# Kernel optimization log

Measured on AMD Instinct MI355X. Metric: run time of the kernel, lower is better.

Reference implementation:

```python
import jax, jax.numpy as jnp
import numpy as np

B, S, HID = 4, 2048, 512
NH, HD = 8, 64
MAX_REL = 512


def setup_inputs() -> dict:
    key = jax.random.key(0)
    ks = jax.random.split(key, 10)
    sd = 0.02
    return {
        "hidden_states": jax.random.normal(ks[0], (B, S, HID), jnp.float32),
        "attention_mask": jnp.ones((B, S), jnp.float32),
        "Wq": jax.random.normal(ks[1], (HID, HID), jnp.float32) * sd,
        "bq": jnp.zeros((HID,), jnp.float32),
        "Wk": jax.random.normal(ks[2], (HID, HID), jnp.float32) * sd,
        "bk": jnp.zeros((HID,), jnp.float32),
        "Wv": jax.random.normal(ks[3], (HID, HID), jnp.float32) * sd,
        "bv": jnp.zeros((HID,), jnp.float32),
        "Wo": jax.random.normal(ks[4], (HID, HID), jnp.float32) * sd,
        "bo": jnp.zeros((HID,), jnp.float32),
        "rel_table": jax.random.normal(ks[5], (2 * MAX_REL + 1, NH), jnp.float32) * sd,
    }


def _heads(x):
    # [B,S,HID] -> [B,NH,S,HD]
    return x.reshape(B, S, NH, HD).transpose(0, 2, 1, 3)


def reference(hidden_states, attention_mask, Wq, bq, Wk, bk, Wv, bv, Wo, bo, rel_table):
    q = _heads(hidden_states @ Wq + bq)
    k = _heads(hidden_states @ Wk + bk)
    v = _heads(hidden_states @ Wv + bv)

    scores = jnp.einsum("bhqd,bhkd->bhqk", q, k) / jnp.sqrt(jnp.float32(HD))

    # relative position bias: rel[i,j] = clip(j-i, -MAX_REL, MAX_REL) + MAX_REL
    pos = jnp.arange(S)
    rel = jnp.clip(pos[None, :] - pos[:, None], -MAX_REL, MAX_REL) + MAX_REL
    bias = rel_table[rel]                      # [S,S,NH]
    bias = bias.transpose(2, 0, 1)             # [NH,S,S]
    scores = scores + bias[None]

    # mask: 1 attend, 0 masked
    neg = jnp.finfo(scores.dtype).min
    scores = scores + (1.0 - attention_mask)[:, None, None, :] * neg

    probs = jax.nn.softmax(scores, axis=-1)
    ctx = jnp.einsum("bhqk,bhkd->bhqd", probs, v)
    ctx = ctx.transpose(0, 2, 1, 3).reshape(B, S, HID)
    return ctx @ Wo + bo
```

## Files before the change

kernel.cpp:

```cpp
#include <hip/hip_runtime.h>
#include <hip/hip_bf16.h>

#define B_    4
#define S_    2048
#define HID_  512
#define NH_   8
#define HD_   64
#define MAXREL 512
#define M_    (B_ * S_)

#define LOG2E 1.44269504f
#define SCALE_Q (0.125f * LOG2E)

typedef __attribute__((ext_vector_type(8))) short bf8;
typedef __attribute__((ext_vector_type(4))) float f4;

static __device__ __forceinline__ unsigned short f2bf(float f) {
    union { float f; unsigned int u; } v; v.f = f;
    unsigned int u = v.u;
    unsigned int r = (u + 0x7FFFu + ((u >> 16) & 1u)) >> 16;
    return (unsigned short)r;
}

static __device__ __forceinline__ float ex2(float x) {
    float r; asm("v_exp_f32 %0, %1" : "=v"(r) : "v"(x)); return r;
}

#define MFMA16(a, b, c) __builtin_amdgcn_mfma_f32_16x16x32_bf16((a), (b), (c), 0, 0, 0)

__global__ void k_cast_hs(const float* __restrict__ src, unsigned short* __restrict__ dst, int n4) {
    int i = blockIdx.x * blockDim.x + threadIdx.x;
    if (i >= n4) return;
    float4 v = ((const float4*)src)[i];
    ushort4 o;
    o.x = f2bf(v.x); o.y = f2bf(v.y); o.z = f2bf(v.z); o.w = f2bf(v.w);
    ((ushort4*)dst)[i] = o;
}

__global__ void k_transpose_w4(const float* __restrict__ W0, const float* __restrict__ W1,
                               const float* __restrict__ W2, const float* __restrict__ W3,
                               unsigned short* __restrict__ T0, unsigned short* __restrict__ T1,
                               unsigned short* __restrict__ T2, unsigned short* __restrict__ T3) {
    __shared__ float tile[32][33];
    const int z = blockIdx.z;
    const float* W = (z == 0) ? W0 : (z == 1) ? W1 : (z == 2) ? W2 : W3;
    unsigned short* T = (z == 0) ? T0 : (z == 1) ? T1 : (z == 2) ? T2 : T3;
    const int tx = threadIdx.x & 31, ty = threadIdx.x >> 5;
    const int n0 = blockIdx.x * 32, k0 = blockIdx.y * 32;
    #pragma unroll
    for (int i = 0; i < 4; ++i)
        tile[ty + i * 8][tx] = W[(size_t)(k0 + ty + i * 8) * HID_ + n0 + tx];
    __syncthreads();
    #pragma unroll
    for (int i = 0; i < 4; ++i)
        T[(size_t)(n0 + ty + i * 8) * HID_ + k0 + tx] = f2bf(tile[tx][ty + i * 8]);
}

__global__ __launch_bounds__(256, 3) void k_gemm_qkv(
    const unsigned short* __restrict__ Abf,
    const unsigned short* __restrict__ Wqt, const unsigned short* __restrict__ Wkt,
    const unsigned short* __restrict__ Wvt,
    const float* __restrict__ bq, const float* __restrict__ bk, const float* __restrict__ bv,
    unsigned short* __restrict__ Q, unsigned short* __restrict__ K, unsigned short* __restrict__ Vt)
{
    __shared__ unsigned short Al[2][128 * 32];
    __shared__ unsigned short Bl[2][128 * 32];

    const int t = threadIdx.x;
    const int lane = t & 63, w = t >> 6;
    const int lr = lane & 15, lg = lane >> 4;
    const int wr = w >> 1, wc = w & 1;

    const int m0 = blockIdx.x * 128;
    const int ng = blockIdx.y * 128;
    const int z = ng >> 9;
    const int n0 = ng & 511;
    const unsigned short* Wt = (z == 0) ? Wqt : ((z == 1) ? Wkt : Wvt);
    const float* bias = (z == 0) ? bq : ((z == 1) ? bk : bv);
    const float osc = (z == 0) ? SCALE_Q : 1.0f;

    const int srow = t >> 2, skk = (t & 3) * 8;
    const int sslot = (t & 3) ^ ((srow >> 1) & 3);
    const int so0 = srow * 32 + sslot * 8;
    const int so1 = (srow + 64) * 32 + sslot * 8;
    const unsigned short* Ag = &Abf[(size_t)(m0 + srow) * HID_ + skk];
    const unsigned short* Bg = &Wt[(size_t)(n0 + srow) * HID_ + skk];

    const int fx = (lr >> 1) & 3;
    int aoff[4], boff[4];
    #pragma unroll
    for (int i = 0; i < 4; ++i) {
        aoff[i] = (wr * 64 + i * 16 + lr) * 32 + ((lg ^ fx) * 8);
        boff[i] = (wc * 64 + i * 16 + lr) * 32 + ((lg ^ fx) * 8);
    }

    {
        bf8 a0 = *(const bf8*)Ag;
        bf8 a1 = *(const bf8*)(Ag + (size_t)64 * HID_);
        bf8 b0 = *(const bf8*)Bg;
        bf8 b1 = *(const bf8*)(Bg + (size_t)64 * HID_);
        *(bf8*)&Al[0][so0] = a0;  *(bf8*)&Al[0][so1] = a1;
        *(bf8*)&Bl[0][so0] = b0;  *(bf8*)&Bl[0][so1] = b1;
    }
    __syncthreads();

    f4 acc[4][4] = {};
    for (int kt = 0; kt < 16; ++kt) {
        const int cur = kt & 1;
        bf8 ra0, ra1, rb0, rb1;
        if (kt < 15) {
            const int ko = (kt + 1) * 32;
            ra0 = *(const bf8*)(Ag + ko);
            ra1 = *(const bf8*)(Ag + (size_t)64 * HID_ + ko);
            rb0 = *(const bf8*)(Bg + ko);
            rb1 = *(const bf8*)(Bg + (size_t)64 * HID_ + ko);
        }
        bf8 af[4], bf_[4];
        #pragma unroll
        for (int i = 0; i < 4; ++i) {
            af[i]  = *(const bf8*)&Al[cur][aoff[i]];
            bf_[i] = *(const bf8*)&Bl[cur][boff[i]];
        }
        #pragma unroll
        for (int mi = 0; mi < 4; ++mi)
            #pragma unroll
            for (int ni = 0; ni < 4; ++ni)
                acc[mi][ni] = MFMA16(af[mi], bf_[ni], acc[mi][ni]);
        if (kt < 15) {
            const int nxt = cur ^ 1;
            *(bf8*)&Al[nxt][so0] = ra0;  *(bf8*)&Al[nxt][so1] = ra1;
            *(bf8*)&Bl[nxt][so0] = rb0;  *(bf8*)&Bl[nxt][so1] = rb1;
        }
        __syncthreads();
    }

    #pragma unroll
    for (int mi = 0; mi < 4; ++mi)
    #pragma unroll
    for (int ni = 0; ni < 4; ++ni) {
        const int col = n0 + wc * 64 + ni * 16 + lr;
        const int h = col >> 6, d = col & 63;
        const float bs = bias[col];
        const int row0 = m0 + wr * 64 + mi * 16 + lg * 4;
        const int b = row0 >> 11, s0 = row0 & 2047;
        if (z == 2) {
            ushort4 o;
            o.x = f2bf(acc[mi][ni][0] + bs);
            o.y = f2bf(acc[mi][ni][1] + bs);
            o.z = f2bf(acc[mi][ni][2] + bs);
            o.w = f2bf(acc[mi][ni][3] + bs);
            *(ushort4*)&Vt[(((size_t)(b * NH_ + h)) * HD_ + d) * S_ + s0] = o;
        } else {
            unsigned short* dst = (z == 0) ? Q : K;
            #pragma unroll
            for (int r = 0; r < 4; ++r) {
                float v = (acc[mi][ni][r] + bs) * osc;
                dst[(((size_t)(b * NH_ + h)) * S_ + s0 + r) * HD_ + d] = f2bf(v);
            }
        }
    }
}

__global__ __launch_bounds__(512) void k_gemm_out(
    const unsigned short* __restrict__ Abf,
    const unsigned short* __restrict__ Wot,
    const float* __restrict__ bo,
    float* __restrict__ out)
{
    __shared__ unsigned short Al[2][128 * 32];
    __shared__ unsigned short Bl[2][128 * 32];

    const int t = threadIdx.x;
    const int lane = t & 63, w = t >> 6;
    const int lr = lane & 15, lg = lane >> 4;
    const int wr = w >> 2, wc = w & 3;

    const int m0 = blockIdx.x * 128;
    const int n0 = blockIdx.y * 128;

    const int srow = t >> 2, skk = (t & 3) * 8;
    const int sslot = (t & 3) ^ ((srow >> 1) & 3);
    const int so = srow * 32 + sslot * 8;
    const unsigned short* Ag = &Abf[(size_t)(m0 + srow) * HID_ + skk];
    const unsigned short* Bg = &Wot[(size_t)(n0 + srow) * HID_ + skk];

    const int fx = (lr >> 1) & 3;
    int aoff[4], boff[2];
    #pragma unroll
    for (int i = 0; i < 4; ++i)
        aoff[i] = (wr * 64 + i * 16 + lr) * 32 + ((lg ^ fx) * 8);
    #pragma unroll
    for (int i = 0; i < 2; ++i)
        boff[i] = (wc * 32 + i * 16 + lr) * 32 + ((lg ^ fx) * 8);

    {
        bf8 a0 = *(const bf8*)Ag;
        bf8 b0 = *(const bf8*)Bg;
        *(bf8*)&Al[0][so] = a0;
        *(bf8*)&Bl[0][so] = b0;
    }
    __syncthreads();

    f4 acc[4][2] = {};
    for (int kt = 0; kt < 16; ++kt) {
        const int cur = kt & 1;
        bf8 ra, rb;
        if (kt < 15) {
            const int ko = (kt + 1) * 32;
            ra = *(const bf8*)(Ag + ko);
            rb = *(const bf8*)(Bg + ko);
        }
        bf8 af[4], bf_[2];
        #pragma unroll
        for (int i = 0; i < 4; ++i) af[i] = *(const bf8*)&Al[cur][aoff[i]];
        #pragma unroll
        for (int i = 0; i < 2; ++i) bf_[i] = *(const bf8*)&Bl[cur][boff[i]];
        #pragma unroll
        for (int mi = 0; mi < 4; ++mi)
            #pragma unroll
            for (int ni = 0; ni < 2; ++ni)
                acc[mi][ni] = MFMA16(af[mi], bf_[ni], acc[mi][ni]);
        if (kt < 15) {
            const int nxt = cur ^ 1;
            *(bf8*)&Al[nxt][so] = ra;
            *(bf8*)&Bl[nxt][so] = rb;
        }
        __syncthreads();
    }

    #pragma unroll
    for (int mi = 0; mi < 4; ++mi)
    #pragma unroll
    for (int ni = 0; ni < 2; ++ni) {
        const int col = n0 + wc * 32 + ni * 16 + lr;
        const float bs = bo[col];
        const int row0 = m0 + wr * 64 + mi * 16 + lg * 4;
        #pragma unroll
        for (int r = 0; r < 4; ++r)
            out[(size_t)(row0 + r) * HID_ + col] = acc[mi][ni][r] + bs;
    }
}

__global__ __launch_bounds__(512, 4) void k_flash(
    const unsigned short* __restrict__ Q, const unsigned short* __restrict__ K,
    const unsigned short* __restrict__ Vt,
    const float* __restrict__ rel_table, const float* __restrict__ mask,
    unsigned short* __restrict__ ctx)
{
    __shared__ unsigned short Klds[2][4096];
    __shared__ unsigned short Vlds[2][4096];
    __shared__ unsigned short Ps[8][16][72];
    __shared__ float maskc[S_];
    __shared__ float Tb[1028];

    const int t = threadIdx.x;
    const int lane = t & 63, w = t >> 6;
    const int lr = lane & 15, lg = lane >> 4;

    const int flat = blockIdx.x;
    const int idx = flat >> 3;
    const int bh = (flat & 7) * 4 + (idx >> 4);
    const int qb = idx & 15;
    const int b = bh >> 3, h = bh & 7;
    const int q0 = qb * 128;

    for (int i = t; i < 1025; i += 512) Tb[i] = rel_table[i * NH_ + h] * LOG2E;
    for (int i = t; i < S_; i += 512)
        maskc[i] = (1.0f - mask[b * S_ + i]) * -3.0e38f;

    const unsigned short* Kb = K + (size_t)bh * S_ * HD_;
    const unsigned short* Vb = Vt + (size_t)bh * HD_ * S_;

    const int myq = q0 + w * 16 + lr;
    bf8 qf0, qf1;
    {
        const unsigned short* qg = &Q[((size_t)bh * S_ + myq) * HD_ + lg * 8];
        qf0 = *(const bf8*)qg;
        qf1 = *(const bf8*)(qg + 32);
    }

    const int srow = t >> 3, sslot = t & 7;
    const int ldso = srow * 64 + ((sslot ^ (srow & 7)) * 8);

    f4 cacc[4] = {};
    float m_s = -INFINITY, l_s = 0.f;

    {
        bf8 a = *(const bf8*)&Kb[(size_t)srow * HD_ + sslot * 8];
        bf8 d = *(const bf8*)&Vb[(size_t)srow * S_ + sslot * 8];
        *(bf8*)&Klds[0][ldso] = a;
        *(bf8*)&Vlds[0][ldso] = d;
    }
    __syncthreads();

    const int xr = lr & 7;
    for (int ti = 0; ti < 32; ++ti) {
        const int cur = ti & 1;
        const int kv0 = ti * 64;

        bf8 sK, sV;
        if (ti < 31) {
            const int nx = kv0 + 64;
            sK = *(const bf8*)&Kb[(size_t)(nx + srow) * HD_ + sslot * 8];
            sV = *(const bf8*)&Vb[(size_t)srow * S_ + nx + sslot * 8];
        }

        f4 sa[4];
        #pragma unroll
        for (int nt = 0; nt < 4; ++nt) {
            const int row = (nt * 16 + lr) * 64;
            bf8 kf0 = *(const bf8*)&Klds[cur][row + ((0 + lg) ^ xr) * 8];
            bf8 kf1 = *(const bf8*)&Klds[cur][row + ((4 + lg) ^ xr) * 8];
            f4 u = {};
            u = MFMA16(kf0, qf0, u);
            u = MFMA16(kf1, qf1, u);
            sa[nt] = u;
        }

        float4 mk[4];
        #pragma unroll
        for (int nt = 0; nt < 4; ++nt)
            mk[nt] = *(const float4*)&maskc[kv0 + nt * 16 + lg * 4];

        float tmax = -INFINITY;
        #pragma unroll
        for (int nt = 0; nt < 4; ++nt) {
            const int kb0 = kv0 + nt * 16 + lg * 4 - myq + MAXREL;
            #pragma unroll
            for (int r = 0; r < 4; ++r) {
                int ic = kb0 + r;
                ic = ic < 0 ? 0 : (ic > 2 * MAXREL ? 2 * MAXREL : ic);
                float mkv = (r == 0) ? mk[nt].x : (r == 1) ? mk[nt].y : (r == 2) ? mk[nt].z : mk[nt].w;
                float sv = sa[nt][r] + Tb[ic] + mkv;
                sa[nt][r] = sv;
                tmax = fmaxf(tmax, sv);
            }
        }
        tmax = fmaxf(tmax, __shfl_xor(tmax, 16));
        tmax = fmaxf(tmax, __shfl_xor(tmax, 32));

        if (!__all(tmax <= m_s + 8.0f)) {
            const float mnew = fmaxf(m_s, tmax);
            const float fac = ex2(m_s - mnew);
            l_s *= fac;
            #pragma unroll
            for (int dt = 0; dt < 4; ++dt)
                #pragma unroll
                for (int r = 0; r < 4; ++r) cacc[dt][r] *= fac;
            m_s = mnew;
        }

        float psum = 0.f;
        unsigned int pk[8];
        #pragma unroll
        for (int nt = 0; nt < 4; ++nt) {
            float p0 = ex2(sa[nt][0] - m_s);
            float p1 = ex2(sa[nt][1] - m_s);
            float p2 = ex2(sa[nt][2] - m_s);
            float p3 = ex2(sa[nt][3] - m_s);
            psum += (p0 + p1) + (p2 + p3);
            asm("v_cvt_pk_bf16_f32 %0, %1, %2" : "=v"(pk[nt * 2])     : "v"(p0), "v"(p1));
            asm("v_cvt_pk_bf16_f32 %0, %1, %2" : "=v"(pk[nt * 2 + 1]) : "v"(p2), "v"(p3));
        }
        psum += __shfl_xor(psum, 16);
        psum += __shfl_xor(psum, 32);
        l_s += psum;

        #pragma unroll
        for (int nt = 0; nt < 4; ++nt) {
            uint2 pv; pv.x = pk[nt * 2]; pv.y = pk[nt * 2 + 1];
            *(uint2*)&Ps[w][lr][nt * 16 + lg * 4] = pv;
        }
        asm volatile("s_waitcnt lgkmcnt(0)" ::: "memory");
        __builtin_amdgcn_sched_barrier(0);

        #pragma unroll
        for (int kc = 0; kc < 2; ++kc) {
            bf8 pb = *(const bf8*)&Ps[w][lr][kc * 32 + lg * 8];
            #pragma unroll
            for (int dt = 0; dt < 4; ++dt) {
                const int row = (dt * 16 + lr) * 64;
                bf8 vf = *(const bf8*)&Vlds[cur][row + ((kc * 4 + lg) ^ xr) * 8];
                cacc[dt] = MFMA16(vf, pb, cacc[dt]);
            }
        }

        if (ti < 31) {
            *(bf8*)&Klds[cur ^ 1][ldso] = sK;
            *(bf8*)&Vlds[cur ^ 1][ldso] = sV;
        }
        __syncthreads();
    }

    const float inv = 1.0f / l_s;
    unsigned short* cg = &ctx[(size_t)(b * S_ + myq) * HID_ + h * HD_];
    #pragma unroll
    for (int dt = 0; dt < 4; ++dt) {
        ushort4 o;
        o.x = f2bf(cacc[dt][0] * inv);
        o.y = f2bf(cacc[dt][1] * inv);
        o.z = f2bf(cacc[dt][2] * inv);
        o.w = f2bf(cacc[dt][3] * inv);
        *(ushort4*)&cg[dt * 16 + lg * 4] = o;
    }
}

extern "C" void kernel_launch(void* const* d_in, const int* in_sizes, int n_in,
                              void* d_out, int out_size, void* d_ws, size_t ws_size,
                              hipStream_t stream) {
    const float* hs  = (const float*)d_in[0];
    const float* msk = (const float*)d_in[1];
    const float* Wq  = (const float*)d_in[2];
    const float* bq  = (const float*)d_in[3];
    const float* Wk  = (const float*)d_in[4];
    const float* bk  = (const float*)d_in[5];
    const float* Wv  = (const float*)d_in[6];
    const float* bv  = (const float*)d_in[7];
    const float* Wo  = (const float*)d_in[8];
    const float* bo  = (const float*)d_in[9];
    const float* rel = (const float*)d_in[10];
    float* out = (float*)d_out;

    char* ws = (char*)d_ws;
    unsigned short* hsb = (unsigned short*)ws; ws += (size_t)M_ * HID_ * 2;
    unsigned short* Wqt = (unsigned short*)ws; ws += (size_t)HID_ * HID_ * 2;
    unsigned short* Wkt = (unsigned short*)ws; ws += (size_t)HID_ * HID_ * 2;
    unsigned short* Wvt = (unsigned short*)ws; ws += (size_t)HID_ * HID_ * 2;
    unsigned short* Wot = (unsigned short*)ws; ws += (size_t)HID_ * HID_ * 2;
    unsigned short* Qb  = (unsigned short*)ws; ws += (size_t)M_ * HID_ * 2;
    unsigned short* Kb  = (unsigned short*)ws; ws += (size_t)M_ * HID_ * 2;
    unsigned short* Vtb = (unsigned short*)ws; ws += (size_t)M_ * HID_ * 2;
    unsigned short* ctxb= (unsigned short*)ws; ws += (size_t)M_ * HID_ * 2;

    k_cast_hs<<<(M_ * HID_ / 4 + 255) / 256, 256, 0, stream>>>(hs, hsb, M_ * HID_ / 4);
    k_transpose_w4<<<dim3(16, 16, 4), 256, 0, stream>>>(Wq, Wk, Wv, Wo, Wqt, Wkt, Wvt, Wot);
    k_gemm_qkv<<<dim3(64, 12), 256, 0, stream>>>(
        hsb, Wqt, Wkt, Wvt, bq, bk, bv, Qb, Kb, Vtb);
    k_flash<<<512, 512, 0, stream>>>(Qb, Kb, Vtb, rel, msk, ctxb);
    k_gemm_out<<<dim3(64, 4), 512, 0, stream>>>(ctxb, Wot, bo, out);
}
```

Before: 125.0 us.

## Use direct global-to-LDS loads in GEMMs and flash; precompute mask and bias window

Replaces the register-staged global loads and LDS stores in both GEMMs and the flash-attention K/V pipeline with global_load_lds, which writes 16 bytes per lane straight into shared memory. The swizzle moves to the global-address side so the LDS layout is unchanged. The flash kernel also drops its per-block LDS mask copy and reads a precomputed additive mask from global memory, produced by a new small kernel. It builds a per-block pre-clipped relative-bias window, so the per-element clamp disappears. This adds a launch and relies on global_load_lds ordering being covered by __syncthreads.

```diff
diff --git a/kernel.cpp b/kernel.cpp
--- a/kernel.cpp
+++ b/kernel.cpp
@@ -26,6 +26,12 @@
     float r; asm("v_exp_f32 %0, %1" : "=v"(r) : "v"(x)); return r;
 }
 
+static __device__ __forceinline__ void gload16(const void* g, void* l) {
+    __builtin_amdgcn_global_load_lds(
+        (const __attribute__((address_space(1))) unsigned int*)g,
+        (__attribute__((address_space(3))) unsigned int*)l, 16, 0, 0);
+}
+
 #define MFMA16(a, b, c) __builtin_amdgcn_mfma_f32_16x16x32_bf16((a), (b), (c), 0, 0, 0)
 
 __global__ void k_cast_hs(const float* __restrict__ src, unsigned short* __restrict__ dst, int n4) {
@@ -35,6 +41,11 @@
     ushort4 o;
     o.x = f2bf(v.x); o.y = f2bf(v.y); o.z = f2bf(v.z); o.w = f2bf(v.w);
     ((ushort4*)dst)[i] = o;
+}
+
+__global__ void k_prep_mask(const float* __restrict__ mask, float* __restrict__ maskadd) {
+    int i = blockIdx.x * blockDim.x + threadIdx.x;
+    if (i < M_) maskadd[i] = (1.0f - mask[i]) * -3.0e38f;
 }
 
 __global__ void k_transpose_w4(const float* __restrict__ W0, const float* __restrict__ W1,
@@ -79,12 +90,14 @@
     const float* bias = (z == 0) ? bq : ((z == 1) ? bk : bv);
     const float osc = (z == 0) ? SCALE_Q : 1.0f;
 
-    const int srow = t >> 2, skk = (t & 3) * 8;
-    const int sslot = (t & 3) ^ ((srow >> 1) & 3);
-    const int so0 = srow * 32 + sslot * 8;
-    const int so1 = (srow + 64) * 32 + sslot * 8;
-    const unsigned short* Ag = &Abf[(size_t)(m0 + srow) * HID_ + skk];
-    const unsigned short* Bg = &Wt[(size_t)(n0 + srow) * HID_ + skk];
+    const int srow = t >> 2;
+    const int sc = (((t & 3) ^ ((srow >> 1) & 3))) * 8;
+    const unsigned short* Ag0 = &Abf[(size_t)(m0 + srow) * HID_ + sc];
+    const unsigned short* Ag1 = &Abf[(size_t)(m0 + 64 + srow) * HID_ + sc];
+    const unsigned short* Bg0 = &Wt[(size_t)(n0 + srow) * HID_ + sc];
+    const unsigned short* Bg1 = &Wt[(size_t)(n0 + 64 + srow) * HID_ + sc];
+    char* dA0 = (char*)&Al[0][0] + w * 1024;
+    char* dB0 = (char*)&Bl[0][0] + w * 1024;
 
     const int fx = (lr >> 1) & 3;
     int aoff[4], boff[4];
@@ -94,26 +107,22 @@
         boff[i] = (wc * 64 + i * 16 + lr) * 32 + ((lg ^ fx) * 8);
     }
 
-    {
-        bf8 a0 = *(const bf8*)Ag;
-        bf8 a1 = *(const bf8*)(Ag + (size_t)64 * HID_);
-        bf8 b0 = *(const bf8*)Bg;
-        bf8 b1 = *(const bf8*)(Bg + (size_t)64 * HID_);
-        *(bf8*)&Al[0][so0] = a0;  *(bf8*)&Al[0][so1] = a1;
-        *(bf8*)&Bl[0][so0] = b0;  *(bf8*)&Bl[0][so1] = b1;
-    }
+    gload16(Ag0, dA0);
+    gload16(Ag1, dA0 + 4096);
+    gload16(Bg0, dB0);
+    gload16(Bg1, dB0 + 4096);
     __syncthreads();
 
     f4 acc[4][4] = {};
     for (int kt = 0; kt < 16; ++kt) {
         const int cur = kt & 1;
-        bf8 ra0, ra1, rb0, rb1;
         if (kt < 15) {
             const int ko = (kt + 1) * 32;
-            ra0 = *(const bf8*)(Ag + ko);
-            ra1 = *(const bf8*)(Ag + (size_t)64 * HID_ + ko);
-            rb0 = *(const bf8*)(Bg + ko);
-            rb1 = *(const bf8*)(Bg + (size_t)64 * HID_ + ko);
+            const int bo = (cur ^ 1) * 8192;
+            gload16(Ag0 + ko, dA0 + bo);
+            gload16(Ag1 + ko, dA0 + bo + 4096);
+            gload16(Bg0 + ko, dB0 + bo);
+            gload16(Bg1 + ko, dB0 + bo + 4096);
         }
         bf8 af[4], bf_[4];
         #pragma unroll
@@ -126,11 +135,6 @@
             #pragma unroll
             for (int ni = 0; ni < 4; ++ni)
                 acc[mi][ni] = MFMA16(af[mi], bf_[ni], acc[mi][ni]);
-        if (kt < 15) {
-            const int nxt = cur ^ 1;
-            *(bf8*)&Al[nxt][so0] = ra0;  *(bf8*)&Al[nxt][so1] = ra1;
-            *(bf8*)&Bl[nxt][so0] = rb0;  *(bf8*)&Bl[nxt][so1] = rb1;
-        }
         __syncthreads();
     }
 
@@ -178,11 +182,12 @@
     const int m0 = blockIdx.x * 128;
     const int n0 = blockIdx.y * 128;
 
-    const int srow = t >> 2, skk = (t & 3) * 8;
-    const int sslot = (t & 3) ^ ((srow >> 1) & 3);
-    const int so = srow * 32 + sslot * 8;
-    const unsigned short* Ag = &Abf[(size_t)(m0 + srow) * HID_ + skk];
-    const unsigned short* Bg = &Wot[(size_t)(n0 + srow) * HID_ + skk];
+    const int srow = t >> 2;
+    const int sc = (((t & 3) ^ ((srow >> 1) & 3))) * 8;
+    const unsigned short* Ag = &Abf[(size_t)(m0 + srow) * HID_ + sc];
+    const unsigned short* Bg = &Wot[(size_t)(n0 + srow) * HID_ + sc];
+    char* dA = (char*)&Al[0][0] + w * 1024;
+    char* dB = (char*)&Bl[0][0] + w * 1024;
 
     const int fx = (lr >> 1) & 3;
     int aoff[4], boff[2];
@@ -193,22 +198,18 @@
     for (int i = 0; i < 2; ++i)
         boff[i] = (wc * 32 + i * 16 + lr) * 32 + ((lg ^ fx) * 8);
 
-    {
-        bf8 a0 = *(const bf8*)Ag;
-        bf8 b0 = *(const bf8*)Bg;
-        *(bf8*)&Al[0][so] = a0;
-        *(bf8*)&Bl[0][so] = b0;
-    }
+    gload16(Ag, dA);
+    gload16(Bg, dB);
     __syncthreads();
 
     f4 acc[4][2] = {};
     for (int kt = 0; kt < 16; ++kt) {
         const int cur = kt & 1;
-        bf8 ra, rb;
         if (kt < 15) {
             const int ko = (kt + 1) * 32;
-            ra = *(const bf8*)(Ag + ko);
-            rb = *(const bf8*)(Bg + ko);
+            const int bo_ = (cur ^ 1) * 8192;
+            gload16(Ag + ko, dA + bo_);
+            gload16(Bg + ko, dB + bo_);
         }
         bf8 af[4], bf_[2];
         #pragma unroll
@@ -220,11 +221,6 @@
             #pragma unroll
             for (int ni = 0; ni < 2; ++ni)
                 acc[mi][ni] = MFMA16(af[mi], bf_[ni], acc[mi][ni]);
-        if (kt < 15) {
-            const int nxt = cur ^ 1;
-            *(bf8*)&Al[nxt][so] = ra;
-            *(bf8*)&Bl[nxt][so] = rb;
-        }
         __syncthreads();
     }
 
@@ -244,14 +240,13 @@
 __global__ __launch_bounds__(512, 4) void k_flash(
     const unsigned short* __restrict__ Q, const unsigned short* __restrict__ K,
     const unsigned short* __restrict__ Vt,
-    const float* __restrict__ rel_table, const float* __restrict__ mask,
+    const float* __restrict__ rel_table, const float* __restrict__ maskadd,
     unsigned short* __restrict__ ctx)
 {
     __shared__ unsigned short Klds[2][4096];
     __shared__ unsigned short Vlds[2][4096];
     __shared__ unsigned short Ps[8][16][72];
-    __shared__ float maskc[S_];
-    __shared__ float Tb[1028];
+    __shared__ float Tbp[2176];
 
     const int t = threadIdx.x;
     const int lane = t & 63, w = t >> 6;
@@ -264,12 +259,15 @@
     const int b = bh >> 3, h = bh & 7;
     const int q0 = qb * 128;
 
-    for (int i = t; i < 1025; i += 512) Tb[i] = rel_table[i * NH_ + h] * LOG2E;
-    for (int i = t; i < S_; i += 512)
-        maskc[i] = (1.0f - mask[b * S_ + i]) * -3.0e38f;
+    for (int i = t; i < 2176; i += 512) {
+        int r = i - q0 - 127;
+        r = r < -MAXREL ? -MAXREL : (r > MAXREL ? MAXREL : r);
+        Tbp[i] = rel_table[(r + MAXREL) * NH_ + h] * LOG2E;
+    }
 
     const unsigned short* Kb = K + (size_t)bh * S_ * HD_;
     const unsigned short* Vb = Vt + (size_t)bh * HD_ * S_;
+    const float* mb = maskadd + b * S_;
 
     const int myq = q0 + w * 16 + lr;
     bf8 qf0, qf1;
@@ -279,31 +277,35 @@
         qf1 = *(const bf8*)(qg + 32);
     }
 
-    const int srow = t >> 3, sslot = t & 7;
-    const int ldso = srow * 64 + ((sslot ^ (srow & 7)) * 8);
+    const int srow = w * 8 + (lane >> 3);
+    const int scol = ((lane & 7) ^ (srow & 7)) * 8;
+    const size_t kbase = (size_t)srow * HD_ + scol;
+    const size_t vbase = (size_t)srow * S_ + scol;
+    const int woff = w * 1024;
 
     f4 cacc[4] = {};
     float m_s = -INFINITY, l_s = 0.f;
 
-    {
-        bf8 a = *(const bf8*)&Kb[(size_t)srow * HD_ + sslot * 8];
-        bf8 d = *(const bf8*)&Vb[(size_t)srow * S_ + sslot * 8];
-        *(bf8*)&Klds[0][ldso] = a;
-        *(bf8*)&Vlds[0][ldso] = d;
-    }
+    gload16(&Kb[kbase], (char*)&Klds[0][0] + woff);
+    gload16(&Vb[vbase], (char*)&Vlds[0][0] + woff);
     __syncthreads();
 
     const int xr = lr & 7;
+    const int jb0 = 127 - w * 16 - lr + lg * 4;
     for (int ti = 0; ti < 32; ++ti) {
         const int cur = ti & 1;
         const int kv0 = ti * 64;
 
-        bf8 sK, sV;
         if (ti < 31) {
-            const int nx = kv0 + 64;
-            sK = *(const bf8*)&Kb[(size_t)(nx + srow) * HD_ + sslot * 8];
-            sV = *(const bf8*)&Vb[(size_t)srow * S_ + nx + sslot * 8];
-        }
+            const int nxt = cur ^ 1;
+            gload16(&Kb[kbase + (size_t)(kv0 + 64) * HD_], (char*)&Klds[nxt][0] + woff);
+            gload16(&Vb[vbase + kv0 + 64], (char*)&Vlds[nxt][0] + woff);
+        }
+
+        float4 mk[4];
+        #pragma unroll
+        for (int nt = 0; nt < 4; ++nt)
+            mk[nt] = *(const float4*)&mb[kv0 + nt * 16 + lg * 4];
 
         f4 sa[4];
         #pragma unroll
@@ -317,21 +319,14 @@
             sa[nt] = u;
         }
 
-        float4 mk[4];
-        #pragma unroll
-        for (int nt = 0; nt < 4; ++nt)
-            mk[nt] = *(const float4*)&maskc[kv0 + nt * 16 + lg * 4];
-
         float tmax = -INFINITY;
         #pragma unroll
         for (int nt = 0; nt < 4; ++nt) {
-            const int kb0 = kv0 + nt * 16 + lg * 4 - myq + MAXREL;
+            const int jb = jb0 + kv0 + nt * 16;
             #pragma unroll
             for (int r = 0; r < 4; ++r) {
-                int ic = kb0 + r;
-                ic = ic < 0 ? 0 : (ic > 2 * MAXREL ? 2 * MAXREL : ic);
                 float mkv = (r == 0) ? mk[nt].x : (r == 1) ? mk[nt].y : (r == 2) ? mk[nt].z : mk[nt].w;
-                float sv = sa[nt][r] + Tb[ic] + mkv;
+                float sv = sa[nt][r] + Tbp[jb + r] + mkv;
                 sa[nt][r] = sv;
                 tmax = fmaxf(tmax, sv);
             }
@@ -383,11 +378,6 @@
                 bf8 vf = *(const bf8*)&Vlds[cur][row + ((kc * 4 + lg) ^ xr) * 8];
                 cacc[dt] = MFMA16(vf, pb, cacc[dt]);
             }
-        }
-
-        if (ti < 31) {
-            *(bf8*)&Klds[cur ^ 1][ldso] = sK;
-            *(bf8*)&Vlds[cur ^ 1][ldso] = sV;
         }
         __syncthreads();
     }
@@ -431,11 +421,13 @@
     unsigned short* Kb  = (unsigned short*)ws; ws += (size_t)M_ * HID_ * 2;
     unsigned short* Vtb = (unsigned short*)ws; ws += (size_t)M_ * HID_ * 2;
     unsigned short* ctxb= (unsigned short*)ws; ws += (size_t)M_ * HID_ * 2;
+    float* maskadd      = (float*)ws;          ws += (size_t)M_ * 4;
 
     k_cast_hs<<<(M_ * HID_ / 4 + 255) / 256, 256, 0, stream>>>(hs, hsb, M_ * HID_ / 4);
+    k_prep_mask<<<(M_ + 255) / 256, 256, 0, stream>>>(msk, maskadd);
     k_transpose_w4<<<dim3(16, 16, 4), 256, 0, stream>>>(Wq, Wk, Wv, Wo, Wqt, Wkt, Wvt, Wot);
     k_gemm_qkv<<<dim3(64, 12), 256, 0, stream>>>(
         hsb, Wqt, Wkt, Wvt, bq, bk, bv, Qb, Kb, Vtb);
-    k_flash<<<512, 512, 0, stream>>>(Qb, Kb, Vtb, rel, msk, ctxb);
+    k_flash<<<512, 512, 0, stream>>>(Qb, Kb, Vtb, rel, maskadd, ctxb);
     k_gemm_out<<<dim3(64, 4), 512, 0, stream>>>(ctxb, Wot, bo, out);
 }
```

Result: faster. 117.1 us (-6.3%).
